# Kernel optimization log

Measured on AMD Instinct MI355X. Metric: run time of the kernel, lower is better.

Reference implementation:

```python
import jax, jax.numpy as jnp
import numpy as np

N, D = 12288, 64


def _ggc(x, adj, W, wih, whh, bih, bhh):
    # Gated graph conv, num_layers=1 (PyG semantics):
    #   m = adj @ (x @ W); x' = GRUCell(m, x)
    m = adj @ (x @ W)                      # [N, D]
    gi = m @ wih.T + bih                   # [N, 3D]
    gh = x @ whh.T + bhh                   # [N, 3D]
    i_r, i_z, i_n = jnp.split(gi, 3, axis=-1)
    h_r, h_z, h_n = jnp.split(gh, 3, axis=-1)
    r = jax.nn.sigmoid(i_r + h_r)
    z = jax.nn.sigmoid(i_z + h_z)
    n = jnp.tanh(i_n + r * h_n)
    return (1.0 - z) * n + z * x


def setup_inputs() -> dict:
    key = jax.random.key(0)
    ks = jax.random.split(key, 8)
    s = 1.0 / np.sqrt(D)
    return {
        "x": jax.random.normal(ks[0], (N, D), jnp.float32),
        "adj": jax.random.uniform(ks[1], (N, N), jnp.float32),
        "W1": jax.random.normal(ks[2], (D, D), jnp.float32) * s,
        "wih1": jax.random.normal(ks[3], (3 * D, D), jnp.float32) * s,
        "whh1": jax.random.normal(ks[4], (3 * D, D), jnp.float32) * s,
        "bih1": jnp.zeros((3 * D,), jnp.float32),
        "bhh1": jnp.zeros((3 * D,), jnp.float32),
        "W2": jax.random.normal(ks[5], (D, D), jnp.float32) * s,
        "wih2": jax.random.normal(ks[6], (3 * D, D), jnp.float32) * s,
        "whh2": jax.random.normal(ks[7], (3 * D, D), jnp.float32) * s,
        "bih2": jnp.zeros((3 * D,), jnp.float32),
        "bhh2": jnp.zeros((3 * D,), jnp.float32),
    }


def reference(x, adj, W1, wih1, whh1, bih1, bhh1, W2, wih2, whh2, bih2, bhh2):
    h = jax.nn.relu(_ggc(x, adj, W1, wih1, whh1, bih1, bhh1))
    # dropout is a no-op in eval mode (training=False)
    return jax.nn.relu(_ggc(h, adj, W2, wih2, whh2, bih2, bhh2))
```

## Files before the change

### kernel.cpp

```cpp
#include <hip/hip_runtime.h>
#include <hip/hip_bf16.h>
#include <cstdint>

#define NN 12288

typedef __attribute__((ext_vector_type(8))) short bfrag8;
typedef __attribute__((ext_vector_type(4))) float f32x4;
typedef __attribute__((ext_vector_type(4))) uint16_t u16x4;
typedef __attribute__((ext_vector_type(8))) uint16_t u16x8;
typedef __attribute__((ext_vector_type(2))) uint32_t u32x2;

__device__ __forceinline__ uint16_t f2bf_rtn(float f) {
    uint32_t u = __float_as_uint(f);
    return (uint16_t)((u + 0x7fffu + ((u >> 16) & 1u)) >> 16);
}
__device__ __forceinline__ void split_bf(float f, uint16_t& hb, uint16_t& lb) {
    uint32_t u = __float_as_uint(f);
    hb = (uint16_t)(u >> 16);
    float fr = f - __uint_as_float(u & 0xffff0000u);
    lb = f2bf_rtn(fr);
}

__device__ __forceinline__ void split4_pk(const f32x4& f, u32x2& hi, u32x2& lo) {
    float2 p01; p01.x = f[0]; p01.y = f[1];
    float2 p23; p23.x = f[2]; p23.y = f[3];
    __hip_bfloat162 h01 = __float22bfloat162_rn(p01);
    __hip_bfloat162 h23 = __float22bfloat162_rn(p23);
    uint32_t uh01 = *reinterpret_cast<uint32_t*>(&h01);
    uint32_t uh23 = *reinterpret_cast<uint32_t*>(&h23);
    float2 r01, r23;
    r01.x = f[0] - __uint_as_float(uh01 << 16);
    r01.y = f[1] - __uint_as_float(uh01 & 0xffff0000u);
    r23.x = f[2] - __uint_as_float(uh23 << 16);
    r23.y = f[3] - __uint_as_float(uh23 & 0xffff0000u);
    __hip_bfloat162 l01 = __float22bfloat162_rn(r01);
    __hip_bfloat162 l23 = __float22bfloat162_rn(r23);
    hi[0] = uh01; hi[1] = uh23;
    lo[0] = *reinterpret_cast<uint32_t*>(&l01);
    lo[1] = *reinterpret_cast<uint32_t*>(&l23);
}

__device__ __forceinline__ void lds_sync() {
    asm volatile("s_waitcnt lgkmcnt(0)" ::: "memory");
    __builtin_amdgcn_s_barrier();
    asm volatile("" ::: "memory");
}

__global__ void wt4_kernel(const float* __restrict__ w0, const float* __restrict__ w1,
                           const float* __restrict__ w2, const float* __restrict__ w3,
                           float* __restrict__ o0, float* __restrict__ o1,
                           float* __restrict__ o2, float* __restrict__ o3) {
    const float* w; float* o;
    switch (blockIdx.y) {
        case 0: w = w0; o = o0; break;
        case 1: w = w1; o = o1; break;
        case 2: w = w2; o = o2; break;
        default: w = w3; o = o3; break;
    }
    int i = blockIdx.x * 256 + threadIdx.x;
    if (i < 192 * 64) {
        int r = i / 64, k = i % 64;
        o[k * 192 + r] = w[i];
    }
}

__global__ void __launch_bounds__(256) xw_kernel(const float* __restrict__ X,
                                                 const float* __restrict__ W,
                                                 uint16_t* __restrict__ Bpk) {
    __shared__ __align__(16) float sW[64 * 65];
    __shared__ __align__(16) float sX[64 * 65];
    const int t = threadIdx.x;
    const int rb = blockIdx.x * 64;
    for (int i = t; i < 4096; i += 256) {
        int rr = i >> 6, cc = i & 63;
        sW[rr * 65 + cc] = W[i];
        sX[rr * 65 + cc] = X[(size_t)rb * 64 + i];
    }
    __syncthreads();
    const int r = t & 63;
    const int c0 = (t >> 6) * 16;
    float acc[16];
#pragma unroll
    for (int i = 0; i < 16; i++) acc[i] = 0.f;
    for (int k = 0; k < 64; k++) {
        float xv = sX[r * 65 + k];
#pragma unroll
        for (int i = 0; i < 16; i++) acc[i] += xv * sW[k * 65 + c0 + i];
    }
    const int j = rb + r;
    const size_t base = (size_t)(j >> 6) * 8192 + (size_t)((j >> 3) & 7) * 512 + (j & 7);
#pragma unroll
    for (int i = 0; i < 16; i++) {
        uint16_t hb, lb;
        split_bf(acc[i], hb, lb);
        size_t idx = base + (size_t)(c0 + i) * 8;
        Bpk[idx] = hb;
        Bpk[idx + 4096] = lb;
    }
}

__global__ void __launch_bounds__(256, 2) spmm_kernel(
    const float* __restrict__ adj,
    const uint16_t* __restrict__ Bpk,
    float* __restrict__ partial,
    int ktiles, int rev) {
    __shared__ __align__(16) uint16_t sAhi[4096];
    __shared__ __align__(16) uint16_t sAlo[4096];
    __shared__ __align__(16) uint16_t sB[8192];
    const int t = threadIdx.x;
    const int rb = blockIdx.x;
    const int kc = blockIdx.y;
    const int tile0 = kc * ktiles;
    const int wave = t >> 6, lane = t & 63;
    const int srow16 = t >> 4;
    const int skk = (t & 15) * 4;
    const float* aptr = adj + (size_t)rb * 64 * NN;
    const int arow = wave * 16 + (lane & 15);
    const int kq = lane >> 4;

    f32x4 acc[4];
#pragma unroll
    for (int i = 0; i < 4; i++) {
        acc[i][0] = 0.f; acc[i][1] = 0.f; acc[i][2] = 0.f; acc[i][3] = 0.f;
    }

    f32x4 lA0[4], lA1[4];
    u16x8 lB0[4], lB1[4];

    auto tid2glob = [&](int i) { return tile0 + (rev ? (ktiles - 1 - i) : i); };

    auto load_tile = [&](int tl, f32x4 (&lA)[4], u16x8 (&lB)[4]) {
        const float* ap = aptr + (size_t)tid2glob(tl) * 64;
#pragma unroll
        for (int it = 0; it < 4; ++it) {
            int row = it * 16 + srow16;
            lA[it] = *(const f32x4*)(ap + (size_t)row * NN + skk);
        }
        const u16x8* bsrc = (const u16x8*)(Bpk + (size_t)tid2glob(tl) * 8192);
#pragma unroll
        for (int i = 0; i < 4; ++i) lB[i] = bsrc[i * 256 + t];
    };

    auto stage_tile = [&](f32x4 (&lA)[4], u16x8 (&lB)[4]) {
#pragma unroll
        for (int it = 0; it < 4; ++it) {
            int row = it * 16 + srow16;
            u32x2 hi, lo;
            split4_pk(lA[it], hi, lo);
            int off = row * 128 + (((skk >> 3) ^ (row & 7)) << 4) + ((skk & 7) << 1);
            *(u32x2*)((char*)sAhi + off) = hi;
            *(u32x2*)((char*)sAlo + off) = lo;
        }
#pragma unroll
        for (int i = 0; i < 4; ++i) ((u16x8*)sB)[i * 256 + t] = lB[i];
    };

    auto compute_tile = [&]() {
#pragma unroll
        for (int ks = 0; ks < 2; ++ks) {
            const int chunk = ks * 4 + kq;
            const int aoff = arow * 128 + ((chunk ^ (arow & 7)) << 4);
            bfrag8 ahi = *(const bfrag8*)((const char*)sAhi + aoff);
            bfrag8 alo = *(const bfrag8*)((const char*)sAlo + aoff);
            const int bko = chunk * 512;
#pragma unroll
            for (int ct = 0; ct < 4; ++ct) {
                int col = ct * 16 + (lane & 15);
                bfrag8 bh = *(const bfrag8*)&sB[bko + col * 8];
                bfrag8 bl = *(const bfrag8*)&sB[4096 + bko + col * 8];
                acc[ct] = __builtin_amdgcn_mfma_f32_16x16x32_bf16(ahi, bh, acc[ct], 0, 0, 0);
                acc[ct] = __builtin_amdgcn_mfma_f32_16x16x32_bf16(alo, bh, acc[ct], 0, 0, 0);
                acc[ct] = __builtin_amdgcn_mfma_f32_16x16x32_bf16(ahi, bl, acc[ct], 0, 0, 0);
            }
        }
    };

    load_tile(0, lA0, lB0);
    load_tile(1, lA1, lB1);

    for (int tl = 0; tl < ktiles; tl += 2) {
        lds_sync();
        stage_tile(lA0, lB0);
        lds_sync();
        if (tl + 2 < ktiles) load_tile(tl + 2, lA0, lB0);
        compute_tile();
        lds_sync();
        stage_tile(lA1, lB1);
        lds_sync();
        if (tl + 3 < ktiles) load_tile(tl + 3, lA1, lB1);
        compute_tile();
    }

    float* pout = partial + (size_t)kc * ((size_t)NN * 64);
    const int orow = rb * 64 + wave * 16 + (lane >> 4) * 4;
    const int ocol = lane & 15;
#pragma unroll
    for (int ct = 0; ct < 4; ++ct) {
#pragma unroll
        for (int r = 0; r < 4; ++r) {
            pout[(size_t)(orow + r) * 64 + ct * 16 + ocol] = acc[ct][r];
        }
    }
}

__global__ void __launch_bounds__(256, 4) gru_kernel(
    const float* __restrict__ partial, int ksplit,
    const float* __restrict__ Xin,
    const float* __restrict__ wtih,
    const float* __restrict__ wthh,
    const float* __restrict__ bih,
    const float* __restrict__ bhh,
    float* __restrict__ hout) {
    __shared__ __align__(16) float sM[32 * 64];
    __shared__ __align__(16) float sX[32 * 64];
    const int t = threadIdx.x;
    const int nb = blockIdx.x * 32;
    {
        size_t g0 = (size_t)nb * 64 + (size_t)t * 8;
        f32x4 s0, s1;
        {
            const f32x4* p0 = (const f32x4*)(partial + g0);
            s0 = p0[0]; s1 = p0[1];
        }
        for (int p = 1; p < ksplit; p++) {
            const f32x4* pp = (const f32x4*)(partial + (size_t)p * ((size_t)NN * 64) + g0);
            f32x4 a = pp[0], b = pp[1];
#pragma unroll
            for (int q = 0; q < 4; q++) { s0[q] += a[q]; s1[q] += b[q]; }
        }
        *(f32x4*)&sM[t * 8] = s0;
        *(f32x4*)&sM[t * 8 + 4] = s1;
        const f32x4* px = (const f32x4*)(Xin + g0);
        *(f32x4*)&sX[t * 8] = px[0];
        *(f32x4*)&sX[t * 8 + 4] = px[1];
    }
    __syncthreads();
    const int wave = t >> 6, lane = t & 63;
    const int nodebase = wave * 8;
    float a_ir[8], a_iz[8], a_in[8], a_hr[8], a_hz[8], a_hn[8];
#pragma unroll
    for (int n = 0; n < 8; n++) {
        a_ir[n] = 0.f; a_iz[n] = 0.f; a_in[n] = 0.f;
        a_hr[n] = 0.f; a_hz[n] = 0.f; a_hn[n] = 0.f;
    }
    for (int k = 0; k < 64; k++) {
        float w0 = wtih[k * 192 + lane];
        float w1 = wtih[k * 192 + 64 + lane];
        float w2 = wtih[k * 192 + 128 + lane];
        float w3 = wthh[k * 192 + lane];
        float w4 = wthh[k * 192 + 64 + lane];
        float w5 = wthh[k * 192 + 128 + lane];
#pragma unroll
        for (int n = 0; n < 8; n++) {
            float mv = sM[(nodebase + n) * 64 + k];
            float xv = sX[(nodebase + n) * 64 + k];
            a_ir[n] += w0 * mv; a_iz[n] += w1 * mv; a_in[n] += w2 * mv;
            a_hr[n] += w3 * xv; a_hz[n] += w4 * xv; a_hn[n] += w5 * xv;
        }
    }
    const float b0 = bih[lane], b1 = bih[64 + lane], b2 = bih[128 + lane];
    const float b3 = bhh[lane], b4 = bhh[64 + lane], b5 = bhh[128 + lane];
#pragma unroll
    for (int n = 0; n < 8; n++) {
        float ir = a_ir[n] + b0, iz = a_iz[n] + b1, inn = a_in[n] + b2;
        float hr = a_hr[n] + b3, hz = a_hz[n] + b4, hn = a_hn[n] + b5;
        float r = 1.f / (1.f + __expf(-(ir + hr)));
        float z = 1.f / (1.f + __expf(-(iz + hz)));
        float nt = tanhf(inn + r * hn);
        float xv = sX[(nodebase + n) * 64 + lane];
        float o = (1.f - z) * nt + z * xv;
        o = fmaxf(o, 0.f);
        size_t oi = (size_t)(nb + nodebase + n) * 64 + lane;
        hout[oi] = o;
    }
}

extern "C" void kernel_launch(void* const* d_in, const int* in_sizes, int n_in,
                              void* d_out, int out_size, void* d_ws, size_t ws_size,
                              hipStream_t stream) {
    const float* x    = (const float*)d_in[0];
    const float* adj  = (const float*)d_in[1];
    const float* W1   = (const float*)d_in[2];
    const float* wih1 = (const float*)d_in[3];
    const float* whh1 = (const float*)d_in[4];
    const float* bih1 = (const float*)d_in[5];
    const float* bhh1 = (const float*)d_in[6];
    const float* W2   = (const float*)d_in[7];
    const float* wih2 = (const float*)d_in[8];
    const float* whh2 = (const float*)d_in[9];
    const float* bih2 = (const float*)d_in[10];
    const float* bhh2 = (const float*)d_in[11];
    float* out = (float*)d_out;

    char* p = (char*)d_ws;
    float* wtih1 = (float*)p; p += (size_t)192 * 64 * 4;
    float* wthh1 = (float*)p; p += (size_t)192 * 64 * 4;
    float* wtih2 = (float*)p; p += (size_t)192 * 64 * 4;
    float* wthh2 = (float*)p; p += (size_t)192 * 64 * 4;
    float* h     = (float*)p; p += (size_t)NN * 64 * 4;
    uint16_t* Bpk = (uint16_t*)p; p += (size_t)NN * 64 * 2 * 2;
    float* partial = (float*)p;
    size_t used = (size_t)(p - (char*)d_ws);
    size_t unit = (size_t)NN * 64 * 4;

    int ksplit = 1;
    const int opts[3] = {4, 2, 1};
    for (int i = 0; i < 3; i++) {
        if (used + (size_t)opts[i] * unit <= ws_size) { ksplit = opts[i]; break; }
    }
    int ktiles = 192 / ksplit;

    wt4_kernel<<<dim3(48, 4), 256, 0, stream>>>(wih1, whh1, wih2, whh2,
                                                wtih1, wthh1, wtih2, wthh2);

    xw_kernel<<<192, 256, 0, stream>>>(x, W1, Bpk);
    spmm_kernel<<<dim3(192, ksplit), 256, 0, stream>>>(adj, Bpk, partial, ktiles, 0);
    gru_kernel<<<384, 256, 0, stream>>>(partial, ksplit, x, wtih1, wthh1, bih1, bhh1, h);
    xw_kernel<<<192, 256, 0, stream>>>(h, W2, Bpk);
    spmm_kernel<<<dim3(192, ksplit), 256, 0, stream>>>(adj, Bpk, partial, ktiles, 1);
    gru_kernel<<<384, 256, 0, stream>>>(partial, ksplit, h, wtih2, wthh2, bih2, bhh2, out);
}
```

Before: 349.2 us.

## Restructure SpMM to two waves with 32-row tiles and double-buffered B

The dense adj @ (xW) kernel drops from 256 to 128 threads per block. Each wave now owns 32 output rows as two 16-row MFMA tiles, so every B fragment read from LDS feeds twice as many MFMAs. B tiles are double-buffered in shared memory, which lets staging of the next tile overlap compute on the current one and cuts the barriers per tile from two to one. A rows are private to each wave, so their single buffer is safe without a barrier. The costs are more registers per thread, more LDS per block, and half as many waves per block to hide global-load latency.

```diff
diff --git a/kernel.cpp b/kernel.cpp
--- a/kernel.cpp
+++ b/kernel.cpp
@@ -99,106 +99,118 @@
     }
 }
 
-__global__ void __launch_bounds__(256, 2) spmm_kernel(
+__global__ void __launch_bounds__(128, 2) spmm_kernel(
     const float* __restrict__ adj,
     const uint16_t* __restrict__ Bpk,
     float* __restrict__ partial,
     int ktiles, int rev) {
     __shared__ __align__(16) uint16_t sAhi[4096];
     __shared__ __align__(16) uint16_t sAlo[4096];
-    __shared__ __align__(16) uint16_t sB[8192];
+    __shared__ __align__(16) uint16_t sB0[8192];
+    __shared__ __align__(16) uint16_t sB1[8192];
     const int t = threadIdx.x;
     const int rb = blockIdx.x;
     const int kc = blockIdx.y;
     const int tile0 = kc * ktiles;
     const int wave = t >> 6, lane = t & 63;
-    const int srow16 = t >> 4;
-    const int skk = (t & 15) * 4;
+    const int srow4 = lane >> 4;
+    const int skk = (lane & 15) * 4;
     const float* aptr = adj + (size_t)rb * 64 * NN;
-    const int arow = wave * 16 + (lane & 15);
     const int kq = lane >> 4;
 
-    f32x4 acc[4];
-#pragma unroll
-    for (int i = 0; i < 4; i++) {
-        acc[i][0] = 0.f; acc[i][1] = 0.f; acc[i][2] = 0.f; acc[i][3] = 0.f;
-    }
-
-    f32x4 lA0[4], lA1[4];
-    u16x8 lB0[4], lB1[4];
+    f32x4 acc[2][4];
+#pragma unroll
+    for (int rt = 0; rt < 2; rt++)
+#pragma unroll
+        for (int ct = 0; ct < 4; ct++) {
+            acc[rt][ct][0] = 0.f; acc[rt][ct][1] = 0.f;
+            acc[rt][ct][2] = 0.f; acc[rt][ct][3] = 0.f;
+        }
+
+    f32x4 aR0[8], aR1[8];
+    u16x8 bR0[8], bR1[8];
 
     auto tid2glob = [&](int i) { return tile0 + (rev ? (ktiles - 1 - i) : i); };
 
-    auto load_tile = [&](int tl, f32x4 (&lA)[4], u16x8 (&lB)[4]) {
-        const float* ap = aptr + (size_t)tid2glob(tl) * 64;
-#pragma unroll
-        for (int it = 0; it < 4; ++it) {
-            int row = it * 16 + srow16;
-            lA[it] = *(const f32x4*)(ap + (size_t)row * NN + skk);
+    auto load_tile = [&](int tl, f32x4 (&aR)[8], u16x8 (&bR)[8]) {
+        const float* ap = aptr + (size_t)tid2glob(tl) * 64 + skk;
+#pragma unroll
+        for (int i = 0; i < 8; ++i) {
+            int row = wave * 32 + i * 4 + srow4;
+            aR[i] = *(const f32x4*)(ap + (size_t)row * NN);
         }
         const u16x8* bsrc = (const u16x8*)(Bpk + (size_t)tid2glob(tl) * 8192);
 #pragma unroll
-        for (int i = 0; i < 4; ++i) lB[i] = bsrc[i * 256 + t];
+        for (int i = 0; i < 8; ++i) bR[i] = bsrc[i * 128 + t];
     };
 
-    auto stage_tile = [&](f32x4 (&lA)[4], u16x8 (&lB)[4]) {
-#pragma unroll
-        for (int it = 0; it < 4; ++it) {
-            int row = it * 16 + srow16;
+    auto stage_tile = [&](f32x4 (&aR)[8], u16x8 (&bR)[8], uint16_t* sB) {
+#pragma unroll
+        for (int i = 0; i < 8; ++i) {
+            int row = wave * 32 + i * 4 + srow4;
             u32x2 hi, lo;
-            split4_pk(lA[it], hi, lo);
+            split4_pk(aR[i], hi, lo);
             int off = row * 128 + (((skk >> 3) ^ (row & 7)) << 4) + ((skk & 7) << 1);
             *(u32x2*)((char*)sAhi + off) = hi;
             *(u32x2*)((char*)sAlo + off) = lo;
         }
 #pragma unroll
-        for (int i = 0; i < 4; ++i) ((u16x8*)sB)[i * 256 + t] = lB[i];
+        for (int i = 0; i < 8; ++i) ((u16x8*)sB)[i * 128 + t] = bR[i];
     };
 
-    auto compute_tile = [&]() {
+    auto compute_tile = [&](const uint16_t* sB) {
 #pragma unroll
         for (int ks = 0; ks < 2; ++ks) {
             const int chunk = ks * 4 + kq;
-            const int aoff = arow * 128 + ((chunk ^ (arow & 7)) << 4);
-            bfrag8 ahi = *(const bfrag8*)((const char*)sAhi + aoff);
-            bfrag8 alo = *(const bfrag8*)((const char*)sAlo + aoff);
             const int bko = chunk * 512;
 #pragma unroll
-            for (int ct = 0; ct < 4; ++ct) {
-                int col = ct * 16 + (lane & 15);
-                bfrag8 bh = *(const bfrag8*)&sB[bko + col * 8];
-                bfrag8 bl = *(const bfrag8*)&sB[4096 + bko + col * 8];
-                acc[ct] = __builtin_amdgcn_mfma_f32_16x16x32_bf16(ahi, bh, acc[ct], 0, 0, 0);
-                acc[ct] = __builtin_amdgcn_mfma_f32_16x16x32_bf16(alo, bh, acc[ct], 0, 0, 0);
-                acc[ct] = __builtin_amdgcn_mfma_f32_16x16x32_bf16(ahi, bl, acc[ct], 0, 0, 0);
+            for (int rt = 0; rt < 2; ++rt) {
+                const int arow = wave * 32 + rt * 16 + (lane & 15);
+                const int aoff = arow * 128 + ((chunk ^ (arow & 7)) << 4);
+                bfrag8 ahi = *(const bfrag8*)((const char*)sAhi + aoff);
+                bfrag8 alo = *(const bfrag8*)((const char*)sAlo + aoff);
+#pragma unroll
+                for (int ct = 0; ct < 4; ++ct) {
+                    int col = ct * 16 + (lane & 15);
+                    bfrag8 bh = *(const bfrag8*)&sB[bko + col * 8];
+                    bfrag8 bl = *(const bfrag8*)&sB[4096 + bko + col * 8];
+                    acc[rt][ct] = __builtin_amdgcn_mfma_f32_16x16x32_bf16(ahi, bh, acc[rt][ct], 0, 0, 0);
+                    acc[rt][ct] = __builtin_amdgcn_mfma_f32_16x16x32_bf16(alo, bh, acc[rt][ct], 0, 0, 0);
+                    acc[rt][ct] = __builtin_amdgcn_mfma_f32_16x16x32_bf16(ahi, bl, acc[rt][ct], 0, 0, 0);
+                }
             }
         }
     };
 
-    load_tile(0, lA0, lB0);
-    load_tile(1, lA1, lB1);
+    load_tile(0, aR0, bR0);
+    load_tile(1, aR1, bR1);
+    stage_tile(aR0, bR0, sB0);
+    lds_sync();
 
     for (int tl = 0; tl < ktiles; tl += 2) {
+        compute_tile(sB0);
+        if (tl + 1 < ktiles) stage_tile(aR1, bR1, sB1);
+        if (tl + 2 < ktiles) load_tile(tl + 2, aR0, bR0);
         lds_sync();
-        stage_tile(lA0, lB0);
-        lds_sync();
-        if (tl + 2 < ktiles) load_tile(tl + 2, lA0, lB0);
-        compute_tile();
-        lds_sync();
-        stage_tile(lA1, lB1);
-        lds_sync();
-        if (tl + 3 < ktiles) load_tile(tl + 3, lA1, lB1);
-        compute_tile();
+        if (tl + 1 < ktiles) {
+            compute_tile(sB1);
+            if (tl + 2 < ktiles) stage_tile(aR0, bR0, sB0);
+            if (tl + 3 < ktiles) load_tile(tl + 3, aR1, bR1);
+            lds_sync();
+        }
     }
 
     float* pout = partial + (size_t)kc * ((size_t)NN * 64);
-    const int orow = rb * 64 + wave * 16 + (lane >> 4) * 4;
     const int ocol = lane & 15;
 #pragma unroll
-    for (int ct = 0; ct < 4; ++ct) {
-#pragma unroll
-        for (int r = 0; r < 4; ++r) {
-            pout[(size_t)(orow + r) * 64 + ct * 16 + ocol] = acc[ct][r];
+    for (int rt = 0; rt < 2; ++rt) {
+        const int orow = rb * 64 + wave * 32 + rt * 16 + (lane >> 4) * 4;
+#pragma unroll
+        for (int ct = 0; ct < 4; ++ct) {
+#pragma unroll
+            for (int r = 0; r < 4; ++r) {
+                pout[(size_t)(orow + r) * 64 + ct * 16 + ocol] = acc[rt][ct][r];
+            }
         }
     }
 }
@@ -314,9 +326,9 @@
                                                 wtih1, wthh1, wtih2, wthh2);
 
     xw_kernel<<<192, 256, 0, stream>>>(x, W1, Bpk);
-    spmm_kernel<<<dim3(192, ksplit), 256, 0, stream>>>(adj, Bpk, partial, ktiles, 0);
+    spmm_kernel<<<dim3(192, ksplit), 128, 0, stream>>>(adj, Bpk, partial, ktiles, 0);
     gru_kernel<<<384, 256, 0, stream>>>(partial, ksplit, x, wtih1, wthh1, bih1, bhh1, h);
     xw_kernel<<<192, 256, 0, stream>>>(h, W2, Bpk);
-    spmm_kernel<<<dim3(192, ksplit), 256, 0, stream>>>(adj, Bpk, partial, ktiles, 1);
+    spmm_kernel<<<dim3(192, ksplit), 128, 0, stream>>>(adj, Bpk, partial, ktiles, 1);
     gru_kernel<<<384, 256, 0, stream>>>(partial, ksplit, h, wtih2, wthh2, bih2, bhh2, out);
 }
```

Result: faster. 336.9 us, median of 2 (-3.5%).

## Replace LDS-staged split-K SpMM with single-wave register-direct dense GEMM

Applied to the files above, without the earlier changes.

The adj@XW kernel now runs one 64-thread wave per 16-row band. Each wave loads its A fragments and the packed B fragments straight from global memory into registers, with a four-deep software pipeline, and does the whole K range itself. This removes the LDS staging, the barriers and the split-K partial buffers plus their reduction in the GRU kernel. The cost is that B is no longer shared across waves through LDS, so each wave re-reads the full packed XW from global or L2. Register pressure also goes up from holding several A and B tiles.

```diff
diff --git a/kernel.cpp b/kernel.cpp
--- a/kernel.cpp
+++ b/kernel.cpp
@@ -3,12 +3,12 @@
 #include <cstdint>
 
 #define NN 12288
+#define NT 192
 
 typedef __attribute__((ext_vector_type(8))) short bfrag8;
 typedef __attribute__((ext_vector_type(4))) float f32x4;
-typedef __attribute__((ext_vector_type(4))) uint16_t u16x4;
-typedef __attribute__((ext_vector_type(8))) uint16_t u16x8;
 typedef __attribute__((ext_vector_type(2))) uint32_t u32x2;
+typedef __attribute__((ext_vector_type(4))) uint32_t u32x4;
 
 __device__ __forceinline__ uint16_t f2bf_rtn(float f) {
     uint32_t u = __float_as_uint(f);
@@ -40,12 +40,6 @@
     lo[1] = *reinterpret_cast<uint32_t*>(&l23);
 }
 
-__device__ __forceinline__ void lds_sync() {
-    asm volatile("s_waitcnt lgkmcnt(0)" ::: "memory");
-    __builtin_amdgcn_s_barrier();
-    asm volatile("" ::: "memory");
-}
-
 __global__ void wt4_kernel(const float* __restrict__ w0, const float* __restrict__ w1,
                            const float* __restrict__ w2, const float* __restrict__ w3,
                            float* __restrict__ o0, float* __restrict__ o1,
@@ -99,24 +93,19 @@
     }
 }
 
-__global__ void __launch_bounds__(256, 2) spmm_kernel(
+struct ATile { f32x4 v[4]; };
+struct BTile { bfrag8 h[2][4]; bfrag8 l[2][4]; };
+
+__global__ void __launch_bounds__(64) spmm_kernel(
     const float* __restrict__ adj,
     const uint16_t* __restrict__ Bpk,
-    float* __restrict__ partial,
-    int ktiles, int rev) {
-    __shared__ __align__(16) uint16_t sAhi[4096];
-    __shared__ __align__(16) uint16_t sAlo[4096];
-    __shared__ __align__(16) uint16_t sB[8192];
-    const int t = threadIdx.x;
-    const int rb = blockIdx.x;
-    const int kc = blockIdx.y;
-    const int tile0 = kc * ktiles;
-    const int wave = t >> 6, lane = t & 63;
-    const int srow16 = t >> 4;
-    const int skk = (t & 15) * 4;
-    const float* aptr = adj + (size_t)rb * 64 * NN;
-    const int arow = wave * 16 + (lane & 15);
+    float* __restrict__ mout,
+    int rev) {
+    const int band = blockIdx.x;
+    const int lane = threadIdx.x;
     const int kq = lane >> 4;
+    const int colb = lane & 15;
+    const float* arow = adj + (size_t)(band * 16 + colb) * NN;
 
     f32x4 acc[4];
 #pragma unroll
@@ -124,87 +113,80 @@
         acc[i][0] = 0.f; acc[i][1] = 0.f; acc[i][2] = 0.f; acc[i][3] = 0.f;
     }
 
-    f32x4 lA0[4], lA1[4];
-    u16x8 lB0[4], lB1[4];
-
-    auto tid2glob = [&](int i) { return tile0 + (rev ? (ktiles - 1 - i) : i); };
-
-    auto load_tile = [&](int tl, f32x4 (&lA)[4], u16x8 (&lB)[4]) {
-        const float* ap = aptr + (size_t)tid2glob(tl) * 64;
-#pragma unroll
-        for (int it = 0; it < 4; ++it) {
-            int row = it * 16 + srow16;
-            lA[it] = *(const f32x4*)(ap + (size_t)row * NN + skk);
-        }
-        const u16x8* bsrc = (const u16x8*)(Bpk + (size_t)tid2glob(tl) * 8192);
-#pragma unroll
-        for (int i = 0; i < 4; ++i) lB[i] = bsrc[i * 256 + t];
+    auto g = [&](int t) { return rev ? (NT - 1 - t) : t; };
+
+    auto load_A = [&](int t, ATile& A) {
+        const float* p = arow + (size_t)g(t) * 64 + kq * 8;
+        A.v[0] = *(const f32x4*)(p);
+        A.v[1] = *(const f32x4*)(p + 4);
+        A.v[2] = *(const f32x4*)(p + 32);
+        A.v[3] = *(const f32x4*)(p + 36);
     };
-
-    auto stage_tile = [&](f32x4 (&lA)[4], u16x8 (&lB)[4]) {
-#pragma unroll
-        for (int it = 0; it < 4; ++it) {
-            int row = it * 16 + srow16;
-            u32x2 hi, lo;
-            split4_pk(lA[it], hi, lo);
-            int off = row * 128 + (((skk >> 3) ^ (row & 7)) << 4) + ((skk & 7) << 1);
-            *(u32x2*)((char*)sAhi + off) = hi;
-            *(u32x2*)((char*)sAlo + off) = lo;
-        }
-#pragma unroll
-        for (int i = 0; i < 4; ++i) ((u16x8*)sB)[i * 256 + t] = lB[i];
+    auto load_B = [&](int t, BTile& B) {
+        const uint16_t* bp = Bpk + (size_t)g(t) * 8192;
+#pragma unroll
+        for (int ks = 0; ks < 2; ++ks) {
+            const int bko = (ks * 4 + kq) * 512;
+#pragma unroll
+            for (int ct = 0; ct < 4; ++ct) {
+                const int off = bko + (ct * 16 + colb) * 8;
+                B.h[ks][ct] = *(const bfrag8*)(bp + off);
+                B.l[ks][ct] = *(const bfrag8*)(bp + 4096 + off);
+            }
+        }
     };
-
-    auto compute_tile = [&]() {
+    auto compute = [&](ATile& A, BTile& B) {
 #pragma unroll
         for (int ks = 0; ks < 2; ++ks) {
-            const int chunk = ks * 4 + kq;
-            const int aoff = arow * 128 + ((chunk ^ (arow & 7)) << 4);
-            bfrag8 ahi = *(const bfrag8*)((const char*)sAhi + aoff);
-            bfrag8 alo = *(const bfrag8*)((const char*)sAlo + aoff);
-            const int bko = chunk * 512;
+            u32x2 h0, l0, h1, l1;
+            split4_pk(A.v[ks * 2], h0, l0);
+            split4_pk(A.v[ks * 2 + 1], h1, l1);
+            u32x4 H, L;
+            H[0] = h0[0]; H[1] = h0[1]; H[2] = h1[0]; H[3] = h1[1];
+            L[0] = l0[0]; L[1] = l0[1]; L[2] = l1[0]; L[3] = l1[1];
+            bfrag8 ah = *(bfrag8*)&H;
+            bfrag8 al = *(bfrag8*)&L;
 #pragma unroll
             for (int ct = 0; ct < 4; ++ct) {
-                int col = ct * 16 + (lane & 15);
-                bfrag8 bh = *(const bfrag8*)&sB[bko + col * 8];
-                bfrag8 bl = *(const bfrag8*)&sB[4096 + bko + col * 8];
-                acc[ct] = __builtin_amdgcn_mfma_f32_16x16x32_bf16(ahi, bh, acc[ct], 0, 0, 0);
-                acc[ct] = __builtin_amdgcn_mfma_f32_16x16x32_bf16(alo, bh, acc[ct], 0, 0, 0);
-                acc[ct] = __builtin_amdgcn_mfma_f32_16x16x32_bf16(ahi, bl, acc[ct], 0, 0, 0);
+                acc[ct] = __builtin_amdgcn_mfma_f32_16x16x32_bf16(ah, B.h[ks][ct], acc[ct], 0, 0, 0);
+                acc[ct] = __builtin_amdgcn_mfma_f32_16x16x32_bf16(al, B.h[ks][ct], acc[ct], 0, 0, 0);
+                acc[ct] = __builtin_amdgcn_mfma_f32_16x16x32_bf16(ah, B.l[ks][ct], acc[ct], 0, 0, 0);
             }
         }
     };
 
-    load_tile(0, lA0, lB0);
-    load_tile(1, lA1, lB1);
-
-    for (int tl = 0; tl < ktiles; tl += 2) {
-        lds_sync();
-        stage_tile(lA0, lB0);
-        lds_sync();
-        if (tl + 2 < ktiles) load_tile(tl + 2, lA0, lB0);
-        compute_tile();
-        lds_sync();
-        stage_tile(lA1, lB1);
-        lds_sync();
-        if (tl + 3 < ktiles) load_tile(tl + 3, lA1, lB1);
-        compute_tile();
-    }
-
-    float* pout = partial + (size_t)kc * ((size_t)NN * 64);
-    const int orow = rb * 64 + wave * 16 + (lane >> 4) * 4;
-    const int ocol = lane & 15;
+    ATile A0, A1, A2, A3;
+    BTile B0, B1;
+    load_A(0, A0); load_A(1, A1); load_A(2, A2); load_A(3, A3);
+    load_B(0, B0); load_B(1, B1);
+
+    for (int t = 0; t < NT; t += 4) {
+        compute(A0, B0);
+        if (t + 4 < NT) load_A(t + 4, A0);
+        if (t + 2 < NT) load_B(t + 2, B0);
+        compute(A1, B1);
+        if (t + 5 < NT) load_A(t + 5, A1);
+        if (t + 3 < NT) load_B(t + 3, B1);
+        compute(A2, B0);
+        if (t + 6 < NT) load_A(t + 6, A2);
+        if (t + 4 < NT) load_B(t + 4, B0);
+        compute(A3, B1);
+        if (t + 7 < NT) load_A(t + 7, A3);
+        if (t + 5 < NT) load_B(t + 5, B1);
+    }
+
+    const int orow0 = band * 16 + (lane >> 4) * 4;
 #pragma unroll
     for (int ct = 0; ct < 4; ++ct) {
 #pragma unroll
         for (int r = 0; r < 4; ++r) {
-            pout[(size_t)(orow + r) * 64 + ct * 16 + ocol] = acc[ct][r];
+            mout[(size_t)(orow0 + r) * 64 + ct * 16 + colb] = acc[ct][r];
         }
     }
 }
 
 __global__ void __launch_bounds__(256, 4) gru_kernel(
-    const float* __restrict__ partial, int ksplit,
+    const float* __restrict__ m_in,
     const float* __restrict__ Xin,
     const float* __restrict__ wtih,
     const float* __restrict__ wthh,
@@ -217,19 +199,9 @@
     const int nb = blockIdx.x * 32;
     {
         size_t g0 = (size_t)nb * 64 + (size_t)t * 8;
-        f32x4 s0, s1;
-        {
-            const f32x4* p0 = (const f32x4*)(partial + g0);
-            s0 = p0[0]; s1 = p0[1];
-        }
-        for (int p = 1; p < ksplit; p++) {
-            const f32x4* pp = (const f32x4*)(partial + (size_t)p * ((size_t)NN * 64) + g0);
-            f32x4 a = pp[0], b = pp[1];
-#pragma unroll
-            for (int q = 0; q < 4; q++) { s0[q] += a[q]; s1[q] += b[q]; }
-        }
-        *(f32x4*)&sM[t * 8] = s0;
-        *(f32x4*)&sM[t * 8 + 4] = s1;
+        const f32x4* pm = (const f32x4*)(m_in + g0);
+        *(f32x4*)&sM[t * 8] = pm[0];
+        *(f32x4*)&sM[t * 8 + 4] = pm[1];
         const f32x4* px = (const f32x4*)(Xin + g0);
         *(f32x4*)&sX[t * 8] = px[0];
         *(f32x4*)&sX[t * 8 + 4] = px[1];
@@ -298,25 +270,16 @@
     float* wtih2 = (float*)p; p += (size_t)192 * 64 * 4;
     float* wthh2 = (float*)p; p += (size_t)192 * 64 * 4;
     float* h     = (float*)p; p += (size_t)NN * 64 * 4;
+    float* m     = (float*)p; p += (size_t)NN * 64 * 4;
     uint16_t* Bpk = (uint16_t*)p; p += (size_t)NN * 64 * 2 * 2;
-    float* partial = (float*)p;
-    size_t used = (size_t)(p - (char*)d_ws);
-    size_t unit = (size_t)NN * 64 * 4;
-
-    int ksplit = 1;
-    const int opts[3] = {4, 2, 1};
-    for (int i = 0; i < 3; i++) {
-        if (used + (size_t)opts[i] * unit <= ws_size) { ksplit = opts[i]; break; }
-    }
-    int ktiles = 192 / ksplit;
 
     wt4_kernel<<<dim3(48, 4), 256, 0, stream>>>(wih1, whh1, wih2, whh2,
                                                 wtih1, wthh1, wtih2, wthh2);
 
     xw_kernel<<<192, 256, 0, stream>>>(x, W1, Bpk);
-    spmm_kernel<<<dim3(192, ksplit), 256, 0, stream>>>(adj, Bpk, partial, ktiles, 0);
-    gru_kernel<<<384, 256, 0, stream>>>(partial, ksplit, x, wtih1, wthh1, bih1, bhh1, h);
+    spmm_kernel<<<768, 64, 0, stream>>>(adj, Bpk, m, 0);
+    gru_kernel<<<384, 256, 0, stream>>>(m, x, wtih1, wthh1, bih1, bhh1, h);
     xw_kernel<<<192, 256, 0, stream>>>(h, W2, Bpk);
-    spmm_kernel<<<dim3(192, ksplit), 256, 0, stream>>>(adj, Bpk, partial, ktiles, 1);
-    gru_kernel<<<384, 256, 0, stream>>>(partial, ksplit, h, wtih2, wthh2, bih2, bhh2, out);
-}
+    spmm_kernel<<<768, 64, 0, stream>>>(adj, Bpk, m, 1);
+    gru_kernel<<<384, 256, 0, stream>>>(m, h, wtih2, wthh2, bih2, bhh2, out);
+}
```

Measured after the change: 508.1 us. 45.5% more time.
